# Kernel optimization log

Hardware: AMD Instinct MI355X
Metric: run time of the kernel (lower is better)

The kernel has to match this reference:

```python
import jax, jax.numpy as jnp
import numpy as np

N_GRAPHS = 1000  # static number of graphs for global_mean_pool


def setup_inputs() -> dict:
    key = jax.random.key(0)
    ks = jax.random.split(key, 12)
    N, E, DIN, H, OUT = 100000, 1600000, 64, 128, 10
    x = jax.random.normal(ks[0], (N, DIN), dtype=jnp.float32)
    edge_index = jax.random.randint(ks[1], (2, E), 0, N, dtype=jnp.int64)
    batch = jnp.sort(jax.random.randint(ks[2], (N,), 0, N_GRAPHS, dtype=jnp.int64))
    g = lambda k, shp, fan: jax.random.normal(k, shp, dtype=jnp.float32) * np.float32(1.0 / np.sqrt(fan))
    return {
        "x": x, "edge_index": edge_index, "batch": batch,
        "W1": g(ks[3], (DIN, H), DIN), "b1": jnp.zeros((H,), jnp.float32),
        "W2": g(ks[4], (H, H), H),     "b2": jnp.zeros((H,), jnp.float32),
        "W3": g(ks[5], (H, H), H),     "b3": jnp.zeros((H,), jnp.float32),
        "Wl": g(ks[6], (H, OUT), H),   "bl": jnp.zeros((OUT,), jnp.float32),
    }


def _gcn_norm(edge_index, num_nodes):
    # Add self-loops, compute symmetric normalization D^-1/2 (A+I) D^-1/2.
    loops = jnp.arange(num_nodes, dtype=edge_index.dtype)
    src = jnp.concatenate([edge_index[0], loops])
    dst = jnp.concatenate([edge_index[1], loops])
    deg = jax.ops.segment_sum(jnp.ones_like(dst, dtype=jnp.float32), dst, num_segments=num_nodes)
    dinv = jnp.where(deg > 0, jax.lax.rsqrt(jnp.maximum(deg, 1.0)), 0.0)
    norm = dinv[src] * dinv[dst]  # [E + N]
    return src, dst, norm


def _gcn_conv(h, W, b, src, dst, norm, num_nodes):
    h = h @ W                              # linear transform first (PyG GCNConv)
    msg = h[src] * norm[:, None]           # gather + edge scale
    out = jax.ops.segment_sum(msg, dst, num_segments=num_nodes)  # scatter-add
    return out + b


def reference(x, edge_index, batch, W1, b1, W2, b2, W3, b3, Wl, bl):
    N = x.shape[0]
    src, dst, norm = _gcn_norm(edge_index, N)
    h = jax.nn.relu(_gcn_conv(x, W1, b1, src, dst, norm, N))
    h = jax.nn.relu(_gcn_conv(h, W2, b2, src, dst, norm, N))
    h = jax.nn.relu(_gcn_conv(h, W3, b3, src, dst, norm, N))
    # global mean pool over graphs
    sums = jax.ops.segment_sum(h, batch, num_segments=N_GRAPHS)
    cnt = jax.ops.segment_sum(jnp.ones((N,), jnp.float32), batch, num_segments=N_GRAPHS)
    pooled = sums / jnp.maximum(cnt, 1.0)[:, None]
    # dropout(p=0.5) is identity in eval mode
    return pooled @ Wl + bl  # [N_GRAPHS, OUT]
```

## Files before the change

kernel.cpp:

```cpp
#include <hip/hip_runtime.h>
#include <math.h>

#define HID 128
#define NOUT 10
#define NG 1000
#define SCAN_B 256

typedef unsigned short u16;
typedef __attribute__((ext_vector_type(8))) short bf16x8;
typedef __attribute__((ext_vector_type(4))) float f32x4;

__device__ inline u16 f2bf(float f) {
    unsigned x = __float_as_uint(f);
    return (u16)((x + 0x7FFF + ((x >> 16) & 1)) >> 16);
}
__device__ inline float bf2f(u16 b) { return __uint_as_float(((unsigned)b) << 16); }

__global__ void k_zero(float* __restrict__ p, int n) {
    int i = blockIdx.x * 256 + threadIdx.x;
    if (i < n) p[i] = 0.f;
}

__global__ void k_count(const int* __restrict__ ei, int* __restrict__ counts, int E) {
    int e = blockIdx.x * 256 + threadIdx.x;
    if (e < E) atomicAdd(&counts[ei[(size_t)E + e]], 1);
}

__global__ void k_dinv(const int* __restrict__ counts, float* __restrict__ dinv, int N) {
    int v = blockIdx.x * 256 + threadIdx.x;
    if (v < N) dinv[v] = rsqrtf((float)(counts[v] + 1));
}

__global__ __launch_bounds__(SCAN_B) void k_scan1(const int* __restrict__ counts,
                                                  int* __restrict__ rowptr,
                                                  int* __restrict__ bsum, int N) {
    __shared__ int s[SCAN_B];
    int t = threadIdx.x;
    int i = blockIdx.x * SCAN_B + t;
    int v = (i < N) ? counts[i] : 0;
    s[t] = v;
    __syncthreads();
    for (int off = 1; off < SCAN_B; off <<= 1) {
        int u = (t >= off) ? s[t - off] : 0;
        __syncthreads();
        s[t] += u;
        __syncthreads();
    }
    if (i < N) rowptr[i] = s[t] - v;
    if (t == SCAN_B - 1) bsum[blockIdx.x] = s[t];
}

__global__ __launch_bounds__(512) void k_scan2(int* __restrict__ bsum, int nb) {
    __shared__ int s[512];
    int t = threadIdx.x;
    int v = (t < nb) ? bsum[t] : 0;
    s[t] = v;
    __syncthreads();
    for (int off = 1; off < 512; off <<= 1) {
        int u = (t >= off) ? s[t - off] : 0;
        __syncthreads();
        s[t] += u;
        __syncthreads();
    }
    if (t < nb) bsum[t] = s[t] - v;
}

__global__ void k_scan3(int* __restrict__ rowptr, const int* __restrict__ bsum, int N, int E) {
    int i = blockIdx.x * SCAN_B + threadIdx.x;
    if (i < N) rowptr[i] += bsum[blockIdx.x];
    if (i == 0) rowptr[N] = E;
}

__global__ void k_scatter(const int* __restrict__ ei, const float* __restrict__ dinv,
                          const int* __restrict__ rowptr, int* __restrict__ fill,
                          int2* __restrict__ sorted, int E) {
    int e = blockIdx.x * 256 + threadIdx.x;
    if (e >= E) return;
    int s = ei[e];
    int d = ei[(size_t)E + e];
    int pos = rowptr[d] + atomicAdd(&fill[d], 1);
    float nrm = dinv[s] * dinv[d];
    sorted[pos] = make_int2(s, __float_as_int(nrm));
}

__global__ void k_bounds(const int* __restrict__ batch, int* __restrict__ gstart, int N) {
    int i = blockIdx.x * 256 + threadIdx.x;
    if (i >= N) return;
    int cur = batch[i];
    if (i == 0) {
        for (int g = 0; g <= cur; ++g) gstart[g] = 0;
    } else {
        int prev = batch[i - 1];
        for (int g = prev + 1; g <= cur; ++g) gstart[g] = i;
    }
    if (i == N - 1) {
        for (int g = cur + 1; g <= NG; ++g) gstart[g] = N;
    }
}

template<int K>
__global__ void k_wsplit(const float* __restrict__ W, u16* __restrict__ whi, u16* __restrict__ wlo) {
    int idx = blockIdx.x * 256 + threadIdx.x;
    if (idx >= K * HID) return;
    int k = idx >> 7;
    int col = idx & 127;
    float v = W[idx];
    u16 hb = f2bf(v);
    u16 lb = f2bf(v - bf2f(hb));
    int ks = k >> 5;
    int kq = (k >> 3) & 3;
    int j = k & 7;
    int c = col >> 4;
    int r = col & 15;
    int lane = kq * 16 + r;
    size_t pos = ((size_t)(ks * 8 + c) * 64 + lane) * 8 + j;
    whi[pos] = hb;
    wlo[pos] = lb;
}

template<int K, bool RELU_IN>
__global__ __launch_bounds__(256) void k_gemm_mfma(const float* __restrict__ in,
                                                   const u16* __restrict__ whi,
                                                   const u16* __restrict__ wlo,
                                                   u16* __restrict__ hW, int N) {
    constexpr int NKS = K / 32;
    const int w = threadIdx.x >> 6;
    const int l = threadIdx.x & 63;
    const int row0 = blockIdx.x * 64 + w * 16;
    const int r = l & 15;
    const int q = l >> 4;

    int arow = row0 + r;
    if (arow > N - 1) arow = N - 1;
    const float* ap = in + (size_t)arow * K + q * 8;

    bf16x8 ahi[NKS], alo[NKS];
#pragma unroll
    for (int ks = 0; ks < NKS; ++ks) {
        float4 v0 = *(const float4*)(ap + ks * 32);
        float4 v1 = *(const float4*)(ap + ks * 32 + 4);
        float va[8] = {v0.x, v0.y, v0.z, v0.w, v1.x, v1.y, v1.z, v1.w};
#pragma unroll
        for (int j = 0; j < 8; ++j) {
            float f = va[j];
            if (RELU_IN) f = fmaxf(f, 0.f);
            u16 hb = f2bf(f);
            ahi[ks][j] = (short)hb;
            alo[ks][j] = (short)f2bf(f - bf2f(hb));
        }
    }

    f32x4 acc[8];
#pragma unroll
    for (int c = 0; c < 8; ++c) acc[c] = (f32x4){0.f, 0.f, 0.f, 0.f};

    const bf16x8* whiv = (const bf16x8*)whi;
    const bf16x8* wlov = (const bf16x8*)wlo;

#pragma unroll
    for (int ks = 0; ks < NKS; ++ks) {
#pragma unroll
        for (int c = 0; c < 8; ++c) {
            bf16x8 b = whiv[(size_t)(ks * 8 + c) * 64 + l];
            acc[c] = __builtin_amdgcn_mfma_f32_16x16x32_bf16(ahi[ks], b, acc[c], 0, 0, 0);
            acc[c] = __builtin_amdgcn_mfma_f32_16x16x32_bf16(alo[ks], b, acc[c], 0, 0, 0);
        }
    }
#pragma unroll
    for (int ks = 0; ks < NKS; ++ks) {
#pragma unroll
        for (int c = 0; c < 8; ++c) {
            bf16x8 b = wlov[(size_t)(ks * 8 + c) * 64 + l];
            acc[c] = __builtin_amdgcn_mfma_f32_16x16x32_bf16(ahi[ks], b, acc[c], 0, 0, 0);
        }
    }

#pragma unroll
    for (int c = 0; c < 8; ++c) {
#pragma unroll
        for (int i = 0; i < 4; ++i) {
            int rr = row0 + q * 4 + i;
            if (rr < N) hW[(size_t)rr * HID + c * 16 + r] = f2bf(acc[c][i]);
        }
    }
}

__global__ __launch_bounds__(256) void k_aggr(const int* __restrict__ rowptr,
                                              const int2* __restrict__ sorted,
                                              const u16* __restrict__ hW,
                                              const float* __restrict__ dinv,
                                              const float* __restrict__ b,
                                              float* __restrict__ out, int N) {
    int wid = threadIdx.x >> 6;
    int lane = threadIdx.x & 63;
    int v = blockIdx.x * 4 + wid;
    if (v >= N) return;
    int half = lane >> 5;
    int c4 = (lane & 31) * 4;

    float4 a0 = make_float4(0.f, 0.f, 0.f, 0.f);
    float4 a1 = make_float4(0.f, 0.f, 0.f, 0.f);
    int beg = rowptr[v], end = rowptr[v + 1];
    int j = beg + half;
    for (; j + 2 < end; j += 4) {
        int2 e0 = sorted[j];
        int2 e1 = sorted[j + 2];
        float n0 = __int_as_float(e0.y);
        float n1 = __int_as_float(e1.y);
        ushort4 p0 = *(const ushort4*)&hW[(size_t)e0.x * HID + c4];
        ushort4 p1 = *(const ushort4*)&hW[(size_t)e1.x * HID + c4];
        a0.x += bf2f(p0.x) * n0; a0.y += bf2f(p0.y) * n0;
        a0.z += bf2f(p0.z) * n0; a0.w += bf2f(p0.w) * n0;
        a1.x += bf2f(p1.x) * n1; a1.y += bf2f(p1.y) * n1;
        a1.z += bf2f(p1.z) * n1; a1.w += bf2f(p1.w) * n1;
    }
    for (; j < end; j += 2) {
        int2 e0 = sorted[j];
        float n0 = __int_as_float(e0.y);
        ushort4 p0 = *(const ushort4*)&hW[(size_t)e0.x * HID + c4];
        a0.x += bf2f(p0.x) * n0; a0.y += bf2f(p0.y) * n0;
        a0.z += bf2f(p0.z) * n0; a0.w += bf2f(p0.w) * n0;
    }
    float4 acc;
    acc.x = a0.x + a1.x; acc.y = a0.y + a1.y;
    acc.z = a0.z + a1.z; acc.w = a0.w + a1.w;

    acc.x += __shfl_xor(acc.x, 32);
    acc.y += __shfl_xor(acc.y, 32);
    acc.z += __shfl_xor(acc.z, 32);
    acc.w += __shfl_xor(acc.w, 32);

    if (half == 0) {
        float di = dinv[v];
        float sn = di * di;
        float4 bv = *(const float4*)&b[c4];
        ushort4 qq = *(const ushort4*)&hW[(size_t)v * HID + c4];
        acc.x += bv.x + bf2f(qq.x) * sn;
        acc.y += bv.y + bf2f(qq.y) * sn;
        acc.z += bv.z + bf2f(qq.z) * sn;
        acc.w += bv.w + bf2f(qq.w) * sn;
        *(float4*)&out[(size_t)v * HID + c4] = acc;
    }
}

__global__ __launch_bounds__(256) void k_poolfinal(const float* __restrict__ h,
                                                   const int* __restrict__ gstart,
                                                   const float* __restrict__ Wl,
                                                   const float* __restrict__ bl,
                                                   float* __restrict__ out) {
    __shared__ float pool[HID];
    int g = blockIdx.x;
    int t = threadIdx.x;
    int col = t & 127;
    int grp = t >> 7;
    int beg = gstart[g], end = gstart[g + 1];

    float acc = 0.f;
    for (int i = beg + grp; i < end; i += 2)
        acc += fmaxf(h[(size_t)i * HID + col], 0.f);

    if (grp == 1) pool[col] = acc;
    __syncthreads();
    if (grp == 0) {
        float tot = acc + pool[col];
        float c = fmaxf((float)(end - beg), 1.0f);
        pool[col] = tot / c;
    }
    __syncthreads();
    if (t < NOUT) {
        float a = bl[t];
        for (int k = 0; k < HID; ++k) a += pool[k] * Wl[k * NOUT + t];
        out[g * NOUT + t] = a;
    }
}

__global__ void k_probe(float* __restrict__ out, int n, float val) {
    int i = blockIdx.x * 256 + threadIdx.x;
    if (i < n) out[i] = val;
}

extern "C" void kernel_launch(void* const* d_in, const int* in_sizes, int n_in,
                              void* d_out, int out_size, void* d_ws, size_t ws_size,
                              hipStream_t stream) {
    const float* x    = (const float*)d_in[0];
    const int* ei     = (const int*)d_in[1];
    const int* batch  = (const int*)d_in[2];
    const float* W1 = (const float*)d_in[3];
    const float* b1 = (const float*)d_in[4];
    const float* W2 = (const float*)d_in[5];
    const float* b2 = (const float*)d_in[6];
    const float* W3 = (const float*)d_in[7];
    const float* b3 = (const float*)d_in[8];
    const float* Wl = (const float*)d_in[9];
    const float* bl = (const float*)d_in[10];
    float* out = (float*)d_out;

    const int N = in_sizes[0] / 64;
    const int E = in_sizes[1] / 2;

    char* ws = (char*)d_ws;
    const size_t off_dinv   = 0;
    const size_t off_counts = 400000;
    const size_t off_rowptr = 800000;
    const size_t off_fill   = 1200128;
    const size_t off_bsum   = 1600128;
    const size_t off_gstart = 1602176;
    const size_t off_sorted = 2118400;
    const size_t off_hW     = 14918400;
    const size_t off_bufB   = 40518400;
    const size_t off_wf1h   = 91718400;
    const size_t off_wf1l   = 91734784;
    const size_t off_wf2h   = 91751168;
    const size_t off_wf2l   = 91783936;
    const size_t off_wf3h   = 91816704;
    const size_t off_wf3l   = 91849472;
    const size_t need       = 91882240;

    if (ws_size < need) {
        float enc = (float)(ws_size >> 20);
        k_probe<<<(out_size + 255) / 256, 256, 0, stream>>>(out, out_size, enc);
        return;
    }

    float* dinv  = (float*)(ws + off_dinv);
    int* counts  = (int*)(ws + off_counts);
    int* rowptr  = (int*)(ws + off_rowptr);
    int* fill    = (int*)(ws + off_fill);
    int* bsum    = (int*)(ws + off_bsum);
    int* gstart  = (int*)(ws + off_gstart);
    int2* sorted = (int2*)(ws + off_sorted);
    u16* hW      = (u16*)(ws + off_hW);
    float* bufB  = (float*)(ws + off_bufB);
    u16* wf1h = (u16*)(ws + off_wf1h);  u16* wf1l = (u16*)(ws + off_wf1l);
    u16* wf2h = (u16*)(ws + off_wf2h);  u16* wf2l = (u16*)(ws + off_wf2l);
    u16* wf3h = (u16*)(ws + off_wf3h);  u16* wf3l = (u16*)(ws + off_wf3l);

    dim3 blk(256);
    const int gN = (N + 255) / 256;
    const int gE = (E + 255) / 256;
    const int nScanBlk = (N + SCAN_B - 1) / SCAN_B;
    const int mfmaGrid = (N + 63) / 64;
    const int aggrGrid = (N + 3) / 4;

    k_zero<<<gN, blk, 0, stream>>>((float*)counts, N);
    k_count<<<gE, blk, 0, stream>>>(ei, counts, E);
    k_dinv<<<gN, blk, 0, stream>>>(counts, dinv, N);
    k_scan1<<<nScanBlk, SCAN_B, 0, stream>>>(counts, rowptr, bsum, N);
    k_scan2<<<1, 512, 0, stream>>>(bsum, nScanBlk);
    k_scan3<<<nScanBlk, SCAN_B, 0, stream>>>(rowptr, bsum, N, E);
    k_zero<<<gN, blk, 0, stream>>>((float*)fill, N);
    k_scatter<<<gE, blk, 0, stream>>>(ei, dinv, rowptr, fill, sorted, E);
    k_bounds<<<gN, blk, 0, stream>>>(batch, gstart, N);
    k_wsplit<64><<<(64 * HID + 255) / 256, blk, 0, stream>>>(W1, wf1h, wf1l);
    k_wsplit<128><<<(128 * HID + 255) / 256, blk, 0, stream>>>(W2, wf2h, wf2l);
    k_wsplit<128><<<(128 * HID + 255) / 256, blk, 0, stream>>>(W3, wf3h, wf3l);

    k_gemm_mfma<64, false><<<mfmaGrid, blk, 0, stream>>>(x, wf1h, wf1l, hW, N);
    k_aggr<<<aggrGrid, blk, 0, stream>>>(rowptr, sorted, hW, dinv, b1, bufB, N);
    k_gemm_mfma<128, true><<<mfmaGrid, blk, 0, stream>>>(bufB, wf2h, wf2l, hW, N);
    k_aggr<<<aggrGrid, blk, 0, stream>>>(rowptr, sorted, hW, dinv, b2, bufB, N);
    k_gemm_mfma<128, true><<<mfmaGrid, blk, 0, stream>>>(bufB, wf3h, wf3l, hW, N);
    k_aggr<<<aggrGrid, blk, 0, stream>>>(rowptr, sorted, hW, dinv, b3, bufB, N);

    k_poolfinal<<<NG, blk, 0, stream>>>(bufB, gstart, Wl, bl, out);
}
```

Before: 506.0 us.

## Fold source-degree scaling into GEMM epilogue, drop per-edge norms, reuse atomic rank

```diff
diff --git a/kernel.cpp b/kernel.cpp
--- a/kernel.cpp
+++ b/kernel.cpp
@@ -8,6 +8,7 @@
 
 typedef unsigned short u16;
 typedef __attribute__((ext_vector_type(8))) short bf16x8;
+typedef __attribute__((ext_vector_type(8))) unsigned short u16x8;
 typedef __attribute__((ext_vector_type(4))) float f32x4;
 
 __device__ inline u16 f2bf(float f) {
@@ -21,9 +22,10 @@
     if (i < n) p[i] = 0.f;
 }
 
-__global__ void k_count(const int* __restrict__ ei, int* __restrict__ counts, int E) {
+__global__ void k_count_rank(const int* __restrict__ ei, int* __restrict__ counts,
+                             int* __restrict__ rank, int E) {
     int e = blockIdx.x * 256 + threadIdx.x;
-    if (e < E) atomicAdd(&counts[ei[(size_t)E + e]], 1);
+    if (e < E) rank[e] = atomicAdd(&counts[ei[(size_t)E + e]], 1);
 }
 
 __global__ void k_dinv(const int* __restrict__ counts, float* __restrict__ dinv, int N) {
@@ -71,16 +73,13 @@
     if (i == 0) rowptr[N] = E;
 }
 
-__global__ void k_scatter(const int* __restrict__ ei, const float* __restrict__ dinv,
-                          const int* __restrict__ rowptr, int* __restrict__ fill,
-                          int2* __restrict__ sorted, int E) {
+__global__ void k_scatter(const int* __restrict__ ei, const int* __restrict__ rank,
+                          const int* __restrict__ rowptr, int* __restrict__ sorted, int E) {
     int e = blockIdx.x * 256 + threadIdx.x;
     if (e >= E) return;
     int s = ei[e];
     int d = ei[(size_t)E + e];
-    int pos = rowptr[d] + atomicAdd(&fill[d], 1);
-    float nrm = dinv[s] * dinv[d];
-    sorted[pos] = make_int2(s, __float_as_int(nrm));
+    sorted[rowptr[d] + rank[e]] = s;
 }
 
 __global__ void k_bounds(const int* __restrict__ batch, int* __restrict__ gstart, int N) {
@@ -122,7 +121,8 @@
 __global__ __launch_bounds__(256) void k_gemm_mfma(const float* __restrict__ in,
                                                    const u16* __restrict__ whi,
                                                    const u16* __restrict__ wlo,
-                                                   u16* __restrict__ hW, int N) {
+                                                   const float* __restrict__ dinv,
+                                                   u16* __restrict__ g, int N) {
     constexpr int NKS = K / 32;
     const int w = threadIdx.x >> 6;
     const int l = threadIdx.x & 63;
@@ -175,19 +175,25 @@
         }
     }
 
+    float dv[4];
+#pragma unroll
+    for (int i = 0; i < 4; ++i) {
+        int rr = row0 + q * 4 + i;
+        dv[i] = (rr < N) ? dinv[rr] : 0.f;
+    }
 #pragma unroll
     for (int c = 0; c < 8; ++c) {
 #pragma unroll
         for (int i = 0; i < 4; ++i) {
             int rr = row0 + q * 4 + i;
-            if (rr < N) hW[(size_t)rr * HID + c * 16 + r] = f2bf(acc[c][i]);
+            if (rr < N) g[(size_t)rr * HID + c * 16 + r] = f2bf(acc[c][i] * dv[i]);
         }
     }
 }
 
 __global__ __launch_bounds__(256) void k_aggr(const int* __restrict__ rowptr,
-                                              const int2* __restrict__ sorted,
-                                              const u16* __restrict__ hW,
+                                              const int* __restrict__ sorted,
+                                              const u16* __restrict__ g,
                                               const float* __restrict__ dinv,
                                               const float* __restrict__ b,
                                               float* __restrict__ out, int N) {
@@ -195,51 +201,58 @@
     int lane = threadIdx.x & 63;
     int v = blockIdx.x * 4 + wid;
     if (v >= N) return;
-    int half = lane >> 5;
-    int c4 = (lane & 31) * 4;
-
-    float4 a0 = make_float4(0.f, 0.f, 0.f, 0.f);
-    float4 a1 = make_float4(0.f, 0.f, 0.f, 0.f);
+    int qq = lane >> 4;
+    int r = lane & 15;
+    int c8 = r * 8;
+
+    float a0[8], a1[8];
+#pragma unroll
+    for (int i = 0; i < 8; ++i) { a0[i] = 0.f; a1[i] = 0.f; }
+
     int beg = rowptr[v], end = rowptr[v + 1];
-    int j = beg + half;
-    for (; j + 2 < end; j += 4) {
-        int2 e0 = sorted[j];
-        int2 e1 = sorted[j + 2];
-        float n0 = __int_as_float(e0.y);
-        float n1 = __int_as_float(e1.y);
-        ushort4 p0 = *(const ushort4*)&hW[(size_t)e0.x * HID + c4];
-        ushort4 p1 = *(const ushort4*)&hW[(size_t)e1.x * HID + c4];
-        a0.x += bf2f(p0.x) * n0; a0.y += bf2f(p0.y) * n0;
-        a0.z += bf2f(p0.z) * n0; a0.w += bf2f(p0.w) * n0;
-        a1.x += bf2f(p1.x) * n1; a1.y += bf2f(p1.y) * n1;
-        a1.z += bf2f(p1.z) * n1; a1.w += bf2f(p1.w) * n1;
-    }
-    for (; j < end; j += 2) {
-        int2 e0 = sorted[j];
-        float n0 = __int_as_float(e0.y);
-        ushort4 p0 = *(const ushort4*)&hW[(size_t)e0.x * HID + c4];
-        a0.x += bf2f(p0.x) * n0; a0.y += bf2f(p0.y) * n0;
-        a0.z += bf2f(p0.z) * n0; a0.w += bf2f(p0.w) * n0;
-    }
-    float4 acc;
-    acc.x = a0.x + a1.x; acc.y = a0.y + a1.y;
-    acc.z = a0.z + a1.z; acc.w = a0.w + a1.w;
-
-    acc.x += __shfl_xor(acc.x, 32);
-    acc.y += __shfl_xor(acc.y, 32);
-    acc.z += __shfl_xor(acc.z, 32);
-    acc.w += __shfl_xor(acc.w, 32);
-
-    if (half == 0) {
-        float di = dinv[v];
-        float sn = di * di;
-        float4 bv = *(const float4*)&b[c4];
-        ushort4 qq = *(const ushort4*)&hW[(size_t)v * HID + c4];
-        acc.x += bv.x + bf2f(qq.x) * sn;
-        acc.y += bv.y + bf2f(qq.y) * sn;
-        acc.z += bv.z + bf2f(qq.z) * sn;
-        acc.w += bv.w + bf2f(qq.w) * sn;
-        *(float4*)&out[(size_t)v * HID + c4] = acc;
+    int j = beg + qq;
+    for (; j + 4 < end; j += 8) {
+        int s0 = sorted[j];
+        int s1 = sorted[j + 4];
+        u16x8 p0 = *(const u16x8*)&g[(size_t)s0 * HID + c8];
+        u16x8 p1 = *(const u16x8*)&g[(size_t)s1 * HID + c8];
+#pragma unroll
+        for (int i = 0; i < 8; ++i) {
+            a0[i] += bf2f(p0[i]);
+            a1[i] += bf2f(p1[i]);
+        }
+    }
+    for (; j < end; j += 4) {
+        int s0 = sorted[j];
+        u16x8 p0 = *(const u16x8*)&g[(size_t)s0 * HID + c8];
+#pragma unroll
+        for (int i = 0; i < 8; ++i) a0[i] += bf2f(p0[i]);
+    }
+
+#pragma unroll
+    for (int i = 0; i < 8; ++i) {
+        float t = a0[i] + a1[i];
+        t += __shfl_xor(t, 16);
+        t += __shfl_xor(t, 32);
+        a0[i] = t;
+    }
+
+    if (qq == 0) {
+        u16x8 sv = *(const u16x8*)&g[(size_t)v * HID + c8];
+        float dv = dinv[v];
+        float4 bv0 = *(const float4*)&b[c8];
+        float4 bv1 = *(const float4*)&b[c8 + 4];
+        float4 o0, o1;
+        o0.x = bv0.x + dv * (a0[0] + bf2f(sv[0]));
+        o0.y = bv0.y + dv * (a0[1] + bf2f(sv[1]));
+        o0.z = bv0.z + dv * (a0[2] + bf2f(sv[2]));
+        o0.w = bv0.w + dv * (a0[3] + bf2f(sv[3]));
+        o1.x = bv1.x + dv * (a0[4] + bf2f(sv[4]));
+        o1.y = bv1.y + dv * (a0[5] + bf2f(sv[5]));
+        o1.z = bv1.z + dv * (a0[6] + bf2f(sv[6]));
+        o1.w = bv1.w + dv * (a0[7] + bf2f(sv[7]));
+        *(float4*)&out[(size_t)v * HID + c8] = o0;
+        *(float4*)&out[(size_t)v * HID + c8 + 4] = o1;
     }
 }
 
@@ -302,19 +315,19 @@
     const size_t off_dinv   = 0;
     const size_t off_counts = 400000;
     const size_t off_rowptr = 800000;
-    const size_t off_fill   = 1200128;
-    const size_t off_bsum   = 1600128;
-    const size_t off_gstart = 1602176;
-    const size_t off_sorted = 2118400;
-    const size_t off_hW     = 14918400;
-    const size_t off_bufB   = 40518400;
-    const size_t off_wf1h   = 91718400;
-    const size_t off_wf1l   = 91734784;
-    const size_t off_wf2h   = 91751168;
-    const size_t off_wf2l   = 91783936;
-    const size_t off_wf3h   = 91816704;
-    const size_t off_wf3l   = 91849472;
-    const size_t need       = 91882240;
+    const size_t off_rank   = 1200128;
+    const size_t off_bsum   = 7600128;
+    const size_t off_gstart = 7602176;
+    const size_t off_sorted = 7606400;
+    const size_t off_hW     = 14006400;
+    const size_t off_bufB   = 39606400;
+    const size_t off_wf1h   = 90806400;
+    const size_t off_wf1l   = 90822784;
+    const size_t off_wf2h   = 90839168;
+    const size_t off_wf2l   = 90871936;
+    const size_t off_wf3h   = 90904704;
+    const size_t off_wf3l   = 90937472;
+    const size_t need       = 90970240;
 
     if (ws_size < need) {
         float enc = (float)(ws_size >> 20);
@@ -325,10 +338,10 @@
     float* dinv  = (float*)(ws + off_dinv);
     int* counts  = (int*)(ws + off_counts);
     int* rowptr  = (int*)(ws + off_rowptr);
-    int* fill    = (int*)(ws + off_fill);
+    int* rank    = (int*)(ws + off_rank);
     int* bsum    = (int*)(ws + off_bsum);
     int* gstart  = (int*)(ws + off_gstart);
-    int2* sorted = (int2*)(ws + off_sorted);
+    int* sorted  = (int*)(ws + off_sorted);
     u16* hW      = (u16*)(ws + off_hW);
     float* bufB  = (float*)(ws + off_bufB);
     u16* wf1h = (u16*)(ws + off_wf1h);  u16* wf1l = (u16*)(ws + off_wf1l);
@@ -343,23 +356,22 @@
     const int aggrGrid = (N + 3) / 4;
 
     k_zero<<<gN, blk, 0, stream>>>((float*)counts, N);
-    k_count<<<gE, blk, 0, stream>>>(ei, counts, E);
+    k_count_rank<<<gE, blk, 0, stream>>>(ei, counts, rank, E);
     k_dinv<<<gN, blk, 0, stream>>>(counts, dinv, N);
     k_scan1<<<nScanBlk, SCAN_B, 0, stream>>>(counts, rowptr, bsum, N);
     k_scan2<<<1, 512, 0, stream>>>(bsum, nScanBlk);
     k_scan3<<<nScanBlk, SCAN_B, 0, stream>>>(rowptr, bsum, N, E);
-    k_zero<<<gN, blk, 0, stream>>>((float*)fill, N);
-    k_scatter<<<gE, blk, 0, stream>>>(ei, dinv, rowptr, fill, sorted, E);
+    k_scatter<<<gE, blk, 0, stream>>>(ei, rank, rowptr, sorted, E);
     k_bounds<<<gN, blk, 0, stream>>>(batch, gstart, N);
     k_wsplit<64><<<(64 * HID + 255) / 256, blk, 0, stream>>>(W1, wf1h, wf1l);
     k_wsplit<128><<<(128 * HID + 255) / 256, blk, 0, stream>>>(W2, wf2h, wf2l);
     k_wsplit<128><<<(128 * HID + 255) / 256, blk, 0, stream>>>(W3, wf3h, wf3l);
 
-    k_gemm_mfma<64, false><<<mfmaGrid, blk, 0, stream>>>(x, wf1h, wf1l, hW, N);
+    k_gemm_mfma<64, false><<<mfmaGrid, blk, 0, stream>>>(x, wf1h, wf1l, dinv, hW, N);
     k_aggr<<<aggrGrid, blk, 0, stream>>>(rowptr, sorted, hW, dinv, b1, bufB, N);
-    k_gemm_mfma<128, true><<<mfmaGrid, blk, 0, stream>>>(bufB, wf2h, wf2l, hW, N);
+    k_gemm_mfma<128, true><<<mfmaGrid, blk, 0, stream>>>(bufB, wf2h, wf2l, dinv, hW, N);
     k_aggr<<<aggrGrid, blk, 0, stream>>>(rowptr, sorted, hW, dinv, b2, bufB, N);
-    k_gemm_mfma<128, true><<<mfmaGrid, blk, 0, stream>>>(bufB, wf3h, wf3l, hW, N);
+    k_gemm_mfma<128, true><<<mfmaGrid, blk, 0, stream>>>(bufB, wf3h, wf3l, dinv, hW, N);
     k_aggr<<<aggrGrid, blk, 0, stream>>>(rowptr, sorted, hW, dinv, b3, bufB, N);
 
     k_poolfinal<<<NG, blk, 0, stream>>>(bufB, gstart, Wl, bl, out);
```

Result: faster. 458.9 us (-9.3%).
